# Kernel tuning notes

Hardware: AMD Instinct MI355X
Metric: run time of the kernel (lower is better)

The kernel has to match this reference:

```python
import jax, jax.numpy as jnp
import numpy as np

B, T, D = 2, 4096, 512
H = 8
HS = D // H  # 64
CTX = 4096


def setup_inputs() -> dict:
    key = jax.random.key(0)
    ks = jax.random.split(key, 10)
    s = lambda fan_in: fan_in ** -0.5
    x = jax.random.normal(ks[0], (B, T, D), dtype=jnp.float32)
    # per-head q/k/v projections (no bias), stacked over heads: [H, D, HS]
    Wq = jax.random.normal(ks[1], (H, D, HS), dtype=jnp.float32) * s(D)
    Wk = jax.random.normal(ks[2], (H, D, HS), dtype=jnp.float32) * s(D)
    Wv = jax.random.normal(ks[3], (H, D, HS), dtype=jnp.float32) * s(D)
    # output projection [D, D] + bias
    Wproj = jax.random.normal(ks[4], (D, D), dtype=jnp.float32) * s(D)
    bproj = jax.random.normal(ks[5], (D,), dtype=jnp.float32) * 0.01
    # feed-forward: D -> 4D -> D
    W1 = jax.random.normal(ks[6], (D, 4 * D), dtype=jnp.float32) * s(D)
    b1 = jax.random.normal(ks[7], (4 * D,), dtype=jnp.float32) * 0.01
    W2 = jax.random.normal(ks[8], (4 * D, D), dtype=jnp.float32) * s(4 * D)
    b2 = jax.random.normal(ks[9], (D,), dtype=jnp.float32) * 0.01
    return {"x": x, "Wq": Wq, "Wk": Wk, "Wv": Wv, "Wproj": Wproj,
            "bproj": bproj, "W1": W1, "b1": b1, "W2": W2, "b2": b2}


def reference(x, Wq, Wk, Wv, Wproj, bproj, W1, b1, W2, b2):
    Bx, Tx, Dx = x.shape
    scale = HS ** -0.5
    # multi-head causal self-attention (naive, full TxT scores as in source)
    q = jnp.einsum('btd,hde->bhte', x, Wq)
    k = jnp.einsum('btd,hde->bhte', x, Wk)
    v = jnp.einsum('btd,hde->bhte', x, Wv)
    wei = jnp.einsum('bhte,bhse->bhts', q, k) * scale  # [B,H,T,T]
    causal = jnp.tril(jnp.ones((Tx, Tx), dtype=bool))
    wei = jnp.where(causal, wei, -jnp.inf)
    wei = jax.nn.softmax(wei, axis=-1)
    attn = jnp.einsum('bhts,bhse->bhte', wei, v)  # [B,H,T,HS]
    # concat heads (cat along last dim == transpose+reshape of stacked heads)
    attn = attn.transpose(0, 2, 1, 3).reshape(Bx, Tx, Dx)
    sa_out = attn @ Wproj + bproj
    x = x + sa_out
    # feed-forward with residual
    h = jax.nn.relu(x @ W1 + b1)
    x = x + (h @ W2 + b2)
    return x
```

## Files before the change

kernel.cpp:

```cpp
#include <hip/hip_runtime.h>


typedef __attribute__((ext_vector_type(8))) short bf16x8;
typedef __attribute__((ext_vector_type(4))) float f32x4;
typedef __attribute__((ext_vector_type(16))) float f32x16;
typedef unsigned short u16;

__device__ __forceinline__ u16 f2bf(float f) {
  union { float f; unsigned int i; } u; u.f = f;
  unsigned int r = u.i + 0x7fffu + ((u.i >> 16) & 1u);
  return (u16)(r >> 16);
}
__device__ __forceinline__ float bf2f(u16 s) {
  union { unsigned int i; float f; } u; u.i = ((unsigned int)s) << 16;
  return u.f;
}
__device__ __forceinline__ void gload16(const void* g, void* l) {
  __builtin_amdgcn_global_load_lds((const __attribute__((address_space(1))) void*)g,
                                   (__attribute__((address_space(3))) void*)l,
                                   16, 0, 0);
}

__device__ __forceinline__ void plswap_u(unsigned &a, unsigned &b) {
#if defined(__has_builtin) && __has_builtin(__builtin_amdgcn_permlane32_swap)
  auto r = __builtin_amdgcn_permlane32_swap(a, b, false, false);
  a = (unsigned)r[0]; b = (unsigned)r[1];
#else
  asm("v_permlane32_swap_b32 %0, %1" : "+v"(a), "+v"(b));
#endif
}
__device__ __forceinline__ void plswap_f(float &a, float &b) {
  unsigned ua = __builtin_bit_cast(unsigned, a), ub = __builtin_bit_cast(unsigned, b);
  plswap_u(ua, ub);
  a = __builtin_bit_cast(float, ua); b = __builtin_bit_cast(float, ub);
}

__device__ __forceinline__ float tsum16(const f32x16 v) {
  float a = v[0] + v[8],  b = v[1] + v[9];
  float c = v[2] + v[10], d = v[3] + v[11];
  float e = v[4] + v[12], f = v[5] + v[13];
  float g = v[6] + v[14], h = v[7] + v[15];
  a += e; b += f; c += g; d += h;
  a += c; b += d;
  return a + b;
}

__global__ __launch_bounds__(256) void prep_kernel(
    const float* __restrict__ x, const float* __restrict__ Wq,
    const float* __restrict__ Wk, const float* __restrict__ Wv,
    const float* __restrict__ Wproj, const float* __restrict__ W1,
    const float* __restrict__ W2, ushort4* __restrict__ xb4,
    u16* __restrict__ wqkv_t, u16* __restrict__ wproj_t,
    u16* __restrict__ w1_t, u16* __restrict__ w2_t) {
  const int i = blockIdx.x;
  if (i >= 3072) {
    int idx = (i - 3072) * 256 + threadIdx.x;
    float4 v = ((const float4*)x)[idx];
    ushort4 o; o.x = f2bf(v.x); o.y = f2bf(v.y); o.z = f2bf(v.z); o.w = f2bf(v.w);
    xb4[idx] = o;
    return;
  }
  const float* in; u16* out; int C, ldo, bx, by;
  if (i < 768) {
    int which = i >> 8, r = i & 255;
    const float* W = which == 0 ? Wq : (which == 1 ? Wk : Wv);
    int bz = r >> 5;
    in = W + bz * 32768;
    out = wqkv_t + which * 262144 + bz * 32768;
    C = 64; ldo = 512; bx = r & 1; by = (r >> 1) & 15;
  } else if (i < 1024) {
    int r = i - 768;
    in = Wproj; out = wproj_t; C = 512; ldo = 512; bx = r & 15; by = r >> 4;
  } else if (i < 2048) {
    int r = i - 1024;
    in = W1; out = w1_t; C = 2048; ldo = 512; bx = r & 63; by = r >> 6;
  } else {
    int r = i - 2048;
    in = W2; out = w2_t; C = 512; ldo = 2048; bx = r & 15; by = r >> 4;
  }
  __shared__ float t[32][33];
  int c0 = bx * 32, r0 = by * 32;
  int tx = threadIdx.x & 31, ty = threadIdx.x >> 5;
#pragma unroll
  for (int k = 0; k < 4; k++)
    t[ty + 8 * k][tx] = in[(long)(r0 + ty + 8 * k) * C + c0 + tx];
  __syncthreads();
#pragma unroll
  for (int k = 0; k < 4; k++)
    out[(long)(c0 + ty + 8 * k) * ldo + r0 + tx] = f2bf(t[tx][ty + 8 * k]);
}

__global__ void transpose_v_kernel(const u16* __restrict__ qkv, u16* __restrict__ vt) {
  __shared__ u16 t[32][33];
  int z = blockIdx.z;
  const u16* in = qkv + (long)(z >> 3) * 4096 * 1536 + 1024 + (z & 7) * 64;
  u16* out = vt + (long)z * 64 * 4096;
  int c0 = blockIdx.x * 32, r0 = blockIdx.y * 32;
  int tx = threadIdx.x & 31, ty = threadIdx.x >> 5;
#pragma unroll
  for (int k = 0; k < 4; k++)
    t[ty + 8 * k][tx] = in[(long)(r0 + ty + 8 * k) * 1536 + c0 + tx];
  __syncthreads();
#pragma unroll
  for (int k = 0; k < 4; k++)
    out[(long)(c0 + ty + 8 * k) * 4096 + r0 + tx] = t[tx][ty + 8 * k];
}

template <int MODE, int BN>
__global__ __launch_bounds__(256) void gemm_bt_kernel(
    const u16* __restrict__ A, const u16* __restrict__ Bt, void* __restrict__ Out,
    const float* __restrict__ bias, const float* __restrict__ resf,
    const u16* __restrict__ resb, int N, int K) {
  __shared__ __align__(16) char As[128 * 128];
  __shared__ __align__(16) char Bs[BN * 128];
  const int tid = threadIdx.x;
  const int lane = tid & 63, w = tid >> 6;
  const int l15 = lane & 15, l4 = lane >> 4;
  const int nx = gridDim.x, nwg = nx * gridDim.y;
  int id = blockIdx.y * nx + blockIdx.x;
  id = (id & 7) * (nwg >> 3) + (id >> 3);
  const long m0 = (long)(id / nx) * 128;
  const long n0 = (long)(id % nx) * BN;
  const int wm = (w >> 1) * 64, wn = (w & 1) * (BN / 2);
  const int NB = BN / 32;

  f32x4 acc[4][NB] = {};

  for (int kt = 0; kt < K; kt += 64) {
#pragma unroll
    for (int i = 0; i < 4; i++) {
      int basechunk = i * 256 + w * 64;
      int chunk = basechunk + lane;
      int row = chunk >> 3, c = chunk & 7;
      int sc = c ^ (row & 7);
      gload16(A + (m0 + row) * K + kt + sc * 8, As + basechunk * 16);
    }
#pragma unroll
    for (int i = 0; i < BN / 32; i++) {
      int basechunk = i * 256 + w * 64;
      int chunk = basechunk + lane;
      int row = chunk >> 3, c = chunk & 7;
      int sc = c ^ (row & 7);
      gload16(Bt + (n0 + row) * K + kt + sc * 8, Bs + basechunk * 16);
    }
    __syncthreads();
#pragma unroll
    for (int kk = 0; kk < 2; kk++) {
      bf16x8 a[4], b[NB];
#pragma unroll
      for (int m = 0; m < 4; m++) {
        int row = wm + m * 16 + l15;
        int ch = (kk * 4 + l4) ^ (row & 7);
        a[m] = *(const bf16x8*)(As + row * 128 + ch * 16);
      }
#pragma unroll
      for (int n = 0; n < NB; n++) {
        int row = wn + n * 16 + l15;
        int ch = (kk * 4 + l4) ^ (row & 7);
        b[n] = *(const bf16x8*)(Bs + row * 128 + ch * 16);
      }
#pragma unroll
      for (int m = 0; m < 4; m++)
#pragma unroll
        for (int n = 0; n < NB; n++)
          acc[m][n] = __builtin_amdgcn_mfma_f32_16x16x32_bf16(a[m], b[n], acc[m][n], 0, 0, 0);
    }
    __syncthreads();
  }

#pragma unroll
  for (int m = 0; m < 4; m++) {
#pragma unroll
    for (int n = 0; n < NB; n++) {
      long gcol = n0 + wn + n * 16 + l15;
#pragma unroll
      for (int r = 0; r < 4; r++) {
        long grow = m0 + wm + m * 16 + l4 * 4 + r;
        float v = acc[m][n][r];
        if (MODE == 0) {
          ((u16*)Out)[grow * N + gcol] = f2bf(v);
        } else if (MODE == 1) {
          v += bias[gcol] + resf[grow * N + gcol];
          ((u16*)Out)[grow * N + gcol] = f2bf(v);
        } else if (MODE == 2) {
          v += bias[gcol];
          v = v > 0.f ? v : 0.f;
          ((u16*)Out)[grow * N + gcol] = f2bf(v);
        } else if (MODE == 3) {
          v += bias[gcol] + bf2f(resb[grow * N + gcol]);
          ((float*)Out)[grow * N + gcol] = v;
        } else {
          if (gcol < 512) v *= 0.18033688f;
          ((u16*)Out)[grow * N + gcol] = f2bf(v);
        }
      }
    }
  }
}

__global__ __launch_bounds__(512, 4) void attn_kernel(
    const u16* __restrict__ qkv, const u16* __restrict__ vt,
    u16* __restrict__ pacc, float* __restrict__ pli) {
  __shared__ __align__(16) char Ks[2][64 * 128];
  __shared__ __align__(16) char Vs[2][64 * 128];
  const int tid = threadIdx.x;
  const int lane = tid & 63, w = tid >> 6;
  const int l31 = lane & 31, l5 = lane >> 5;

  const int g = blockIdx.x;

  for (int it = 0; it < 2; ++it) {
    const int item = it ? 1023 - g : g;
    const int qt = item >> 6;
    const int bh = (item >> 2) & 15;
    const int qq = item & 3;
    const int b = bh >> 3, h = bh & 7;
    const int qt0 = qt * 256;
    const int L = qt + 1;
    const int j0 = qq * L, j1 = j0 + L;
    const int jdiag = 4 * qt;
    const u16* qbase = qkv + (long)b * 4096 * 1536 + h * 64;
    const u16* kbase = qbase + 512;
    const u16* vtbase = vt + (long)bh * 64 * 4096;

    const int qrow_g = qt0 + w * 32 + l31;
    bf16x8 aq[4];
    {
      const u16* qp = qbase + (long)qrow_g * 1536 + l5 * 8;
#pragma unroll
      for (int kk = 0; kk < 4; kk++) aq[kk] = *(const bf16x8*)(qp + kk * 16);
    }

    const int srow = tid >> 3, sc = (tid & 7) ^ (srow & 7);
    const u16* kp = kbase + (long)(j0 * 64 + srow) * 1536 + sc * 8;
    const u16* vp = vtbase + (long)srow * 4096 + j0 * 64 + sc * 8;
    gload16(kp, Ks[0] + w * 1024);
    gload16(vp, Vs[0] + w * 1024);
    __syncthreads();

    f32x16 oacc[2] = {};
    float li = 0.f;

    for (int j = j0; j < j1; ++j) {
      const int cur = (j - j0) & 1;
      if (j + 1 < j1) {
        kp += 64 * 1536;
        vp += 64;
        gload16(kp, Ks[cur ^ 1] + w * 1024);
        gload16(vp, Vs[cur ^ 1] + w * 1024);
      }

      const bool diag = (j >= jdiag);
      const int thr = qrow_g - j * 64;

#pragma unroll
      for (int n = 0; n < 2; n++) {
        f32x16 st = {};
        __builtin_amdgcn_s_setprio(1);
#pragma unroll
        for (int kk = 0; kk < 4; kk++) {
          int ch = ((l5 + 2 * kk) ^ (l31 & 7)) * 16;
          bf16x8 ak = *(const bf16x8*)(Ks[cur] + (n * 32 + l31) * 128 + ch);
          st = __builtin_amdgcn_mfma_f32_32x32x16_bf16(ak, aq[kk], st, 0, 0, 0);
        }
        __builtin_amdgcn_s_setprio(0);

        if (diag) {
#pragma unroll
          for (int reg = 0; reg < 16; reg++) {
            int key = n * 32 + 4 * l5 + (reg & 3) + 8 * (reg >> 2);
            if (key > thr) st[reg] = -1e30f;
          }
        }

#pragma unroll
        for (int reg = 0; reg < 16; reg++)
          st[reg] = exp2f(st[reg]);
        li += tsum16(st);

#pragma unroll
        for (int jj = 0; jj < 2; jj++) {
          unsigned w0, w1, w2, w3;
          {
            unsigned pa, pb;
            asm("v_cvt_pk_bf16_f32 %0, %1, %2" : "=v"(pa) : "v"(st[(2 * jj) * 4 + 0]), "v"(st[(2 * jj) * 4 + 1]));
            asm("v_cvt_pk_bf16_f32 %0, %1, %2" : "=v"(pb) : "v"(st[(2 * jj + 1) * 4 + 0]), "v"(st[(2 * jj + 1) * 4 + 1]));
            plswap_u(pa, pb);
            w0 = pa; w2 = pb;
          }
          {
            unsigned pa, pb;
            asm("v_cvt_pk_bf16_f32 %0, %1, %2" : "=v"(pa) : "v"(st[(2 * jj) * 4 + 2]), "v"(st[(2 * jj) * 4 + 3]));
            asm("v_cvt_pk_bf16_f32 %0, %1, %2" : "=v"(pb) : "v"(st[(2 * jj + 1) * 4 + 2]), "v"(st[(2 * jj + 1) * 4 + 3]));
            plswap_u(pa, pb);
            w1 = pa; w3 = pb;
          }
          union { unsigned u[4]; bf16x8 v; } bp;
          bp.u[0] = w0; bp.u[1] = w1; bp.u[2] = w2; bp.u[3] = w3;
          int s = 2 * n + jj;
          int ch = ((l5 + 2 * s) ^ (l31 & 7)) * 16;
          bf16x8 av0 = *(const bf16x8*)(Vs[cur] + l31 * 128 + ch);
          bf16x8 av1 = *(const bf16x8*)(Vs[cur] + (32 + l31) * 128 + ch);
          __builtin_amdgcn_s_setprio(1);
          oacc[0] = __builtin_amdgcn_mfma_f32_32x32x16_bf16(av0, bp.v, oacc[0], 0, 0, 0);
          oacc[1] = __builtin_amdgcn_mfma_f32_32x32x16_bf16(av1, bp.v, oacc[1], 0, 0, 0);
          __builtin_amdgcn_s_setprio(0);
        }
      }
      __syncthreads();
    }

    {
      float ta = li, tb = li;
      plswap_f(ta, tb);
      li = ta + tb;
    }

    u16* pa = pacc + (long)item * 16384;
#pragma unroll
    for (int ne = 0; ne < 2; ne++)
#pragma unroll
      for (int gg = 0; gg < 4; gg++) {
        ushort4 o;
        o.x = f2bf(oacc[ne][4 * gg + 0]);
        o.y = f2bf(oacc[ne][4 * gg + 1]);
        o.z = f2bf(oacc[ne][4 * gg + 2]);
        o.w = f2bf(oacc[ne][4 * gg + 3]);
        *(ushort4*)(pa + (w * 32 + l31) * 64 + ne * 32 + 4 * l5 + 8 * gg) = o;
      }
    if (l5 == 0) pli[(long)item * 256 + w * 32 + l31] = li;
  }
}

__global__ __launch_bounds__(256) void attn_merge_kernel(
    const u16* __restrict__ pacc, const float* __restrict__ pli, u16* __restrict__ attnb) {
  int tile = blockIdx.x;
  int qt = tile >> 4, bh = tile & 15;
  int b = bh >> 3, h = bh & 7;
  int ibase = qt * 64 + bh * 4;
  const u16* pq[4];
  const float* lq[4];
#pragma unroll
  for (int q = 0; q < 4; q++) {
    pq[q] = pacc + (long)(ibase + q) * 16384;
    lq[q] = pli + (long)(ibase + q) * 256;
  }
  int t = threadIdx.x;
  int cg = (t & 15) * 4;
  int rsub = t >> 4;
#pragma unroll
  for (int pass = 0; pass < 16; ++pass) {
    int row = pass * 16 + rsub;
    float denom = lq[0][row] + lq[1][row] + lq[2][row] + lq[3][row];
    float acc0 = 0.f, acc1 = 0.f, acc2 = 0.f, acc3 = 0.f;
#pragma unroll
    for (int q = 0; q < 4; q++) {
      ushort4 u = *(const ushort4*)(pq[q] + row * 64 + cg);
      acc0 += bf2f(u.x);
      acc1 += bf2f(u.y);
      acc2 += bf2f(u.z);
      acc3 += bf2f(u.w);
    }
    float inv = 1.f / denom;
    ushort4 o;
    o.x = f2bf(acc0 * inv);
    o.y = f2bf(acc1 * inv);
    o.z = f2bf(acc2 * inv);
    o.w = f2bf(acc3 * inv);
    *(ushort4*)(attnb + ((long)(b * 4096 + qt * 256 + row)) * 512 + h * 64 + cg) = o;
  }
}

extern "C" void kernel_launch(void* const* d_in, const int* in_sizes, int n_in,
                              void* d_out, int out_size, void* d_ws, size_t ws_size,
                              hipStream_t stream) {
  const float* x = (const float*)d_in[0];
  const float* Wq = (const float*)d_in[1];
  const float* Wk = (const float*)d_in[2];
  const float* Wv = (const float*)d_in[3];
  const float* Wproj = (const float*)d_in[4];
  const float* bproj = (const float*)d_in[5];
  const float* W1 = (const float*)d_in[6];
  const float* b1 = (const float*)d_in[7];
  const float* W2 = (const float*)d_in[8];
  const float* b2 = (const float*)d_in[9];

  char* ws = (char*)d_ws;
  u16* xb      = (u16*)(ws);
  u16* wqkv_t  = (u16*)(ws + 8388608);
  u16* wproj_t = (u16*)(ws + 9961472);
  u16* w1_t    = (u16*)(ws + 10485760);
  u16* w2_t    = (u16*)(ws + 12582912);
  u16* qkv     = (u16*)(ws + 14680064);
  u16* vt      = (u16*)(ws + 39845888);
  u16* attnb   = (u16*)(ws + 48234496);
  u16* x1b     = (u16*)(ws + 56623104);
  u16* hbuf    = (u16*)(ws + 65011712);
  float* pli   = (float*)(ws + 56623104 + 2097152);
  u16* pacc    = (u16*)(ws + 65011712);

  prep_kernel<<<7168, 256, 0, stream>>>(x, Wq, Wk, Wv, Wproj, W1, W2,
                                        (ushort4*)xb, wqkv_t, wproj_t, w1_t, w2_t);

  gemm_bt_kernel<4, 128><<<dim3(12, 64), 256, 0, stream>>>(xb, wqkv_t, qkv, nullptr, nullptr, nullptr, 1536, 512);
  transpose_v_kernel<<<dim3(2, 128, 16), 256, 0, stream>>>(qkv, vt);
  attn_kernel<<<512, 512, 0, stream>>>(qkv, vt, pacc, pli);
  attn_merge_kernel<<<256, 256, 0, stream>>>(pacc, pli, attnb);
  gemm_bt_kernel<1, 64><<<dim3(8, 64), 256, 0, stream>>>(attnb, wproj_t, x1b, bproj, x, nullptr, 512, 512);
  gemm_bt_kernel<2, 128><<<dim3(16, 64), 256, 0, stream>>>(x1b, w1_t, hbuf, b1, nullptr, nullptr, 2048, 512);
  gemm_bt_kernel<3, 64><<<dim3(8, 64), 256, 0, stream>>>(hbuf, w2_t, d_out, b2, nullptr, x1b, 512, 2048);
}
```

Baseline: 184.5 us.

## Fuse V transpose into QKV GEMM epilogue and launch one attention item per block

The QKV GEMM epilogue now writes V columns directly in transposed per-head layout, so the separate transpose_v kernel launch and its extra read/write pass over V go away. The attention kernel now launches 1024 blocks with one work item each instead of 512 blocks looping over two paired items. The block-to-item mapping interleaves long and short query tiles for load balance. The V stores in the GEMM epilogue are strided across rows, which may be less coalesced than the old tiled transpose.

Measured after the change: 193.6 us. 4.9% more time.

```diff
diff --git a/kernel.cpp b/kernel.cpp
--- a/kernel.cpp
+++ b/kernel.cpp
@@ -90,27 +90,11 @@
     out[(long)(c0 + ty + 8 * k) * ldo + r0 + tx] = f2bf(t[tx][ty + 8 * k]);
 }
 
-__global__ void transpose_v_kernel(const u16* __restrict__ qkv, u16* __restrict__ vt) {
-  __shared__ u16 t[32][33];
-  int z = blockIdx.z;
-  const u16* in = qkv + (long)(z >> 3) * 4096 * 1536 + 1024 + (z & 7) * 64;
-  u16* out = vt + (long)z * 64 * 4096;
-  int c0 = blockIdx.x * 32, r0 = blockIdx.y * 32;
-  int tx = threadIdx.x & 31, ty = threadIdx.x >> 5;
-#pragma unroll
-  for (int k = 0; k < 4; k++)
-    t[ty + 8 * k][tx] = in[(long)(r0 + ty + 8 * k) * 1536 + c0 + tx];
-  __syncthreads();
-#pragma unroll
-  for (int k = 0; k < 4; k++)
-    out[(long)(c0 + ty + 8 * k) * 4096 + r0 + tx] = t[tx][ty + 8 * k];
-}
-
 template <int MODE, int BN>
 __global__ __launch_bounds__(256) void gemm_bt_kernel(
     const u16* __restrict__ A, const u16* __restrict__ Bt, void* __restrict__ Out,
     const float* __restrict__ bias, const float* __restrict__ resf,
-    const u16* __restrict__ resb, int N, int K) {
+    const u16* __restrict__ resb, u16* __restrict__ vtOut, int N, int K) {
   __shared__ __align__(16) char As[128 * 128];
   __shared__ __align__(16) char Bs[BN * 128];
   const int tid = threadIdx.x;
@@ -173,25 +157,43 @@
 #pragma unroll
     for (int n = 0; n < NB; n++) {
       long gcol = n0 + wn + n * 16 + l15;
-#pragma unroll
-      for (int r = 0; r < 4; r++) {
-        long grow = m0 + wm + m * 16 + l4 * 4 + r;
-        float v = acc[m][n][r];
-        if (MODE == 0) {
-          ((u16*)Out)[grow * N + gcol] = f2bf(v);
-        } else if (MODE == 1) {
-          v += bias[gcol] + resf[grow * N + gcol];
-          ((u16*)Out)[grow * N + gcol] = f2bf(v);
-        } else if (MODE == 2) {
-          v += bias[gcol];
-          v = v > 0.f ? v : 0.f;
-          ((u16*)Out)[grow * N + gcol] = f2bf(v);
-        } else if (MODE == 3) {
-          v += bias[gcol] + bf2f(resb[grow * N + gcol]);
-          ((float*)Out)[grow * N + gcol] = v;
+      if (MODE == 4) {
+        long grow0 = m0 + wm + m * 16 + l4 * 4;
+        if (gcol < 1024) {
+          const float s = (gcol < 512) ? 0.18033688f : 1.0f;
+#pragma unroll
+          for (int r = 0; r < 4; r++)
+            ((u16*)Out)[(grow0 + r) * N + gcol] = f2bf(acc[m][n][r] * s);
         } else {
-          if (gcol < 512) v *= 0.18033688f;
-          ((u16*)Out)[grow * N + gcol] = f2bf(v);
+          int bb = (int)(grow0 >> 12);
+          long trow0 = grow0 & 4095;
+          int hc = (int)(gcol - 1024);
+          int bhh = bb * 8 + (hc >> 6), e = hc & 63;
+          ushort4 o;
+          o.x = f2bf(acc[m][n][0]);
+          o.y = f2bf(acc[m][n][1]);
+          o.z = f2bf(acc[m][n][2]);
+          o.w = f2bf(acc[m][n][3]);
+          *(ushort4*)(vtOut + (long)bhh * 262144 + (long)e * 4096 + trow0) = o;
+        }
+      } else {
+#pragma unroll
+        for (int r = 0; r < 4; r++) {
+          long grow = m0 + wm + m * 16 + l4 * 4 + r;
+          float v = acc[m][n][r];
+          if (MODE == 0) {
+            ((u16*)Out)[grow * N + gcol] = f2bf(v);
+          } else if (MODE == 1) {
+            v += bias[gcol] + resf[grow * N + gcol];
+            ((u16*)Out)[grow * N + gcol] = f2bf(v);
+          } else if (MODE == 2) {
+            v += bias[gcol];
+            v = v > 0.f ? v : 0.f;
+            ((u16*)Out)[grow * N + gcol] = f2bf(v);
+          } else {
+            v += bias[gcol] + bf2f(resb[grow * N + gcol]);
+            ((float*)Out)[grow * N + gcol] = v;
+          }
         }
       }
     }
@@ -208,128 +210,126 @@
   const int l31 = lane & 31, l5 = lane >> 5;
 
   const int g = blockIdx.x;
-
-  for (int it = 0; it < 2; ++it) {
-    const int item = it ? 1023 - g : g;
-    const int qt = item >> 6;
-    const int bh = (item >> 2) & 15;
-    const int qq = item & 3;
-    const int b = bh >> 3, h = bh & 7;
-    const int qt0 = qt * 256;
-    const int L = qt + 1;
-    const int j0 = qq * L, j1 = j0 + L;
-    const int jdiag = 4 * qt;
-    const u16* qbase = qkv + (long)b * 4096 * 1536 + h * 64;
-    const u16* kbase = qbase + 512;
-    const u16* vtbase = vt + (long)bh * 64 * 4096;
-
-    const int qrow_g = qt0 + w * 32 + l31;
-    bf16x8 aq[4];
-    {
-      const u16* qp = qbase + (long)qrow_g * 1536 + l5 * 8;
-#pragma unroll
-      for (int kk = 0; kk < 4; kk++) aq[kk] = *(const bf16x8*)(qp + kk * 16);
-    }
-
-    const int srow = tid >> 3, sc = (tid & 7) ^ (srow & 7);
-    const u16* kp = kbase + (long)(j0 * 64 + srow) * 1536 + sc * 8;
-    const u16* vp = vtbase + (long)srow * 4096 + j0 * 64 + sc * 8;
-    gload16(kp, Ks[0] + w * 1024);
-    gload16(vp, Vs[0] + w * 1024);
+  const int s_ = g >> 8, r_ = g & 255, t_ = r_ >> 4, u_ = r_ & 15;
+  const int qt = (s_ & 1) ? 15 - t_ : t_;
+  const int sub = (s_ << 4) | u_;
+  const int item = qt * 64 + sub;
+  const int bh = sub >> 2, qq = sub & 3;
+  const int b = bh >> 3, h = bh & 7;
+  const int qt0 = qt * 256;
+  const int L = qt + 1;
+  const int j0 = qq * L, j1 = j0 + L;
+  const int jdiag = 4 * qt;
+  const u16* qbase = qkv + (long)b * 4096 * 1536 + h * 64;
+  const u16* kbase = qbase + 512;
+  const u16* vtbase = vt + (long)bh * 64 * 4096;
+
+  const int qrow_g = qt0 + w * 32 + l31;
+  bf16x8 aq[4];
+  {
+    const u16* qp = qbase + (long)qrow_g * 1536 + l5 * 8;
+#pragma unroll
+    for (int kk = 0; kk < 4; kk++) aq[kk] = *(const bf16x8*)(qp + kk * 16);
+  }
+
+  const int srow = tid >> 3, sc = (tid & 7) ^ (srow & 7);
+  const u16* kp = kbase + (long)(j0 * 64 + srow) * 1536 + sc * 8;
+  const u16* vp = vtbase + (long)srow * 4096 + j0 * 64 + sc * 8;
+  gload16(kp, Ks[0] + w * 1024);
+  gload16(vp, Vs[0] + w * 1024);
+  __syncthreads();
+
+  f32x16 oacc[2] = {};
+  float li = 0.f;
+
+  for (int j = j0; j < j1; ++j) {
+    const int cur = (j - j0) & 1;
+    if (j + 1 < j1) {
+      kp += 64 * 1536;
+      vp += 64;
+      gload16(kp, Ks[cur ^ 1] + w * 1024);
+      gload16(vp, Vs[cur ^ 1] + w * 1024);
+    }
+
+    const bool diag = (j >= jdiag);
+    const int thr = qrow_g - j * 64;
+
+#pragma unroll
+    for (int n = 0; n < 2; n++) {
+      f32x16 st = {};
+      __builtin_amdgcn_s_setprio(1);
+#pragma unroll
+      for (int kk = 0; kk < 4; kk++) {
+        int ch = ((l5 + 2 * kk) ^ (l31 & 7)) * 16;
+        bf16x8 ak = *(const bf16x8*)(Ks[cur] + (n * 32 + l31) * 128 + ch);
+        st = __builtin_amdgcn_mfma_f32_32x32x16_bf16(ak, aq[kk], st, 0, 0, 0);
+      }
+      __builtin_amdgcn_s_setprio(0);
+
+      if (diag) {
+#pragma unroll
+        for (int reg = 0; reg < 16; reg++) {
+          int key = n * 32 + 4 * l5 + (reg & 3) + 8 * (reg >> 2);
+          if (key > thr) st[reg] = -1e30f;
+        }
+      }
+
+#pragma unroll
+      for (int reg = 0; reg < 16; reg++)
+        st[reg] = exp2f(st[reg]);
+      li += tsum16(st);
+
+#pragma unroll
+      for (int jj = 0; jj < 2; jj++) {
+        unsigned w0, w1, w2, w3;
+        {
+          unsigned pa, pb;
+          asm("v_cvt_pk_bf16_f32 %0, %1, %2" : "=v"(pa) : "v"(st[(2 * jj) * 4 + 0]), "v"(st[(2 * jj) * 4 + 1]));
+          asm("v_cvt_pk_bf16_f32 %0, %1, %2" : "=v"(pb) : "v"(st[(2 * jj + 1) * 4 + 0]), "v"(st[(2 * jj + 1) * 4 + 1]));
+          plswap_u(pa, pb);
+          w0 = pa; w2 = pb;
+        }
+        {
+          unsigned pa, pb;
+          asm("v_cvt_pk_bf16_f32 %0, %1, %2" : "=v"(pa) : "v"(st[(2 * jj) * 4 + 2]), "v"(st[(2 * jj) * 4 + 3]));
+          asm("v_cvt_pk_bf16_f32 %0, %1, %2" : "=v"(pb) : "v"(st[(2 * jj + 1) * 4 + 2]), "v"(st[(2 * jj + 1) * 4 + 3]));
+          plswap_u(pa, pb);
+          w1 = pa; w3 = pb;
+        }
+        union { unsigned u[4]; bf16x8 v; } bp;
+        bp.u[0] = w0; bp.u[1] = w1; bp.u[2] = w2; bp.u[3] = w3;
+        int s2 = 2 * n + jj;
+        int ch = ((l5 + 2 * s2) ^ (l31 & 7)) * 16;
+        bf16x8 av0 = *(const bf16x8*)(Vs[cur] + l31 * 128 + ch);
+        bf16x8 av1 = *(const bf16x8*)(Vs[cur] + (32 + l31) * 128 + ch);
+        __builtin_amdgcn_s_setprio(1);
+        oacc[0] = __builtin_amdgcn_mfma_f32_32x32x16_bf16(av0, bp.v, oacc[0], 0, 0, 0);
+        oacc[1] = __builtin_amdgcn_mfma_f32_32x32x16_bf16(av1, bp.v, oacc[1], 0, 0, 0);
+        __builtin_amdgcn_s_setprio(0);
+      }
+    }
     __syncthreads();
-
-    f32x16 oacc[2] = {};
-    float li = 0.f;
-
-    for (int j = j0; j < j1; ++j) {
-      const int cur = (j - j0) & 1;
-      if (j + 1 < j1) {
-        kp += 64 * 1536;
-        vp += 64;
-        gload16(kp, Ks[cur ^ 1] + w * 1024);
-        gload16(vp, Vs[cur ^ 1] + w * 1024);
-      }
-
-      const bool diag = (j >= jdiag);
-      const int thr = qrow_g - j * 64;
-
-#pragma unroll
-      for (int n = 0; n < 2; n++) {
-        f32x16 st = {};
-        __builtin_amdgcn_s_setprio(1);
-#pragma unroll
-        for (int kk = 0; kk < 4; kk++) {
-          int ch = ((l5 + 2 * kk) ^ (l31 & 7)) * 16;
-          bf16x8 ak = *(const bf16x8*)(Ks[cur] + (n * 32 + l31) * 128 + ch);
-          st = __builtin_amdgcn_mfma_f32_32x32x16_bf16(ak, aq[kk], st, 0, 0, 0);
-        }
-        __builtin_amdgcn_s_setprio(0);
-
-        if (diag) {
-#pragma unroll
-          for (int reg = 0; reg < 16; reg++) {
-            int key = n * 32 + 4 * l5 + (reg & 3) + 8 * (reg >> 2);
-            if (key > thr) st[reg] = -1e30f;
-          }
-        }
-
-#pragma unroll
-        for (int reg = 0; reg < 16; reg++)
-          st[reg] = exp2f(st[reg]);
-        li += tsum16(st);
-
-#pragma unroll
-        for (int jj = 0; jj < 2; jj++) {
-          unsigned w0, w1, w2, w3;
-          {
-            unsigned pa, pb;
-            asm("v_cvt_pk_bf16_f32 %0, %1, %2" : "=v"(pa) : "v"(st[(2 * jj) * 4 + 0]), "v"(st[(2 * jj) * 4 + 1]));
-            asm("v_cvt_pk_bf16_f32 %0, %1, %2" : "=v"(pb) : "v"(st[(2 * jj + 1) * 4 + 0]), "v"(st[(2 * jj + 1) * 4 + 1]));
-            plswap_u(pa, pb);
-            w0 = pa; w2 = pb;
-          }
-          {
-            unsigned pa, pb;
-            asm("v_cvt_pk_bf16_f32 %0, %1, %2" : "=v"(pa) : "v"(st[(2 * jj) * 4 + 2]), "v"(st[(2 * jj) * 4 + 3]));
-            asm("v_cvt_pk_bf16_f32 %0, %1, %2" : "=v"(pb) : "v"(st[(2 * jj + 1) * 4 + 2]), "v"(st[(2 * jj + 1) * 4 + 3]));
-            plswap_u(pa, pb);
-            w1 = pa; w3 = pb;
-          }
-          union { unsigned u[4]; bf16x8 v; } bp;
-          bp.u[0] = w0; bp.u[1] = w1; bp.u[2] = w2; bp.u[3] = w3;
-          int s = 2 * n + jj;
-          int ch = ((l5 + 2 * s) ^ (l31 & 7)) * 16;
-          bf16x8 av0 = *(const bf16x8*)(Vs[cur] + l31 * 128 + ch);
-          bf16x8 av1 = *(const bf16x8*)(Vs[cur] + (32 + l31) * 128 + ch);
-          __builtin_amdgcn_s_setprio(1);
-          oacc[0] = __builtin_amdgcn_mfma_f32_32x32x16_bf16(av0, bp.v, oacc[0], 0, 0, 0);
-          oacc[1] = __builtin_amdgcn_mfma_f32_32x32x16_bf16(av1, bp.v, oacc[1], 0, 0, 0);
-          __builtin_amdgcn_s_setprio(0);
-        }
-      }
-      __syncthreads();
-    }
-
-    {
-      float ta = li, tb = li;
-      plswap_f(ta, tb);
-      li = ta + tb;
-    }
-
-    u16* pa = pacc + (long)item * 16384;
-#pragma unroll
-    for (int ne = 0; ne < 2; ne++)
-#pragma unroll
-      for (int gg = 0; gg < 4; gg++) {
-        ushort4 o;
-        o.x = f2bf(oacc[ne][4 * gg + 0]);
-        o.y = f2bf(oacc[ne][4 * gg + 1]);
-        o.z = f2bf(oacc[ne][4 * gg + 2]);
-        o.w = f2bf(oacc[ne][4 * gg + 3]);
-        *(ushort4*)(pa + (w * 32 + l31) * 64 + ne * 32 + 4 * l5 + 8 * gg) = o;
-      }
-    if (l5 == 0) pli[(long)item * 256 + w * 32 + l31] = li;
-  }
+  }
+
+  {
+    float ta = li, tb = li;
+    plswap_f(ta, tb);
+    li = ta + tb;
+  }
+
+  u16* pa = pacc + (long)item * 16384;
+#pragma unroll
+  for (int ne = 0; ne < 2; ne++)
+#pragma unroll
+    for (int gg = 0; gg < 4; gg++) {
+      ushort4 o;
+      o.x = f2bf(oacc[ne][4 * gg + 0]);
+      o.y = f2bf(oacc[ne][4 * gg + 1]);
+      o.z = f2bf(oacc[ne][4 * gg + 2]);
+      o.w = f2bf(oacc[ne][4 * gg + 3]);
+      *(ushort4*)(pa + (w * 32 + l31) * 64 + ne * 32 + 4 * l5 + 8 * gg) = o;
+    }
+  if (l5 == 0) pli[(long)item * 256 + w * 32 + l31] = li;
 }
 
 __global__ __launch_bounds__(256) void attn_merge_kernel(
@@ -402,11 +402,10 @@
   prep_kernel<<<7168, 256, 0, stream>>>(x, Wq, Wk, Wv, Wproj, W1, W2,
                                         (ushort4*)xb, wqkv_t, wproj_t, w1_t, w2_t);
 
-  gemm_bt_kernel<4, 128><<<dim3(12, 64), 256, 0, stream>>>(xb, wqkv_t, qkv, nullptr, nullptr, nullptr, 1536, 512);
-  transpose_v_kernel<<<dim3(2, 128, 16), 256, 0, stream>>>(qkv, vt);
-  attn_kernel<<<512, 512, 0, stream>>>(qkv, vt, pacc, pli);
+  gemm_bt_kernel<4, 128><<<dim3(12, 64), 256, 0, stream>>>(xb, wqkv_t, qkv, nullptr, nullptr, nullptr, vt, 1536, 512);
+  attn_kernel<<<1024, 512, 0, stream>>>(qkv, vt, pacc, pli);
   attn_merge_kernel<<<256, 256, 0, stream>>>(pacc, pli, attnb);
-  gemm_bt_kernel<1, 64><<<dim3(8, 64), 256, 0, stream>>>(attnb, wproj_t, x1b, bproj, x, nullptr, 512, 512);
-  gemm_bt_kernel<2, 128><<<dim3(16, 64), 256, 0, stream>>>(x1b, w1_t, hbuf, b1, nullptr, nullptr, 2048, 512);
-  gemm_bt_kernel<3, 64><<<dim3(8, 64), 256, 0, stream>>>(hbuf, w2_t, d_out, b2, nullptr, x1b, 512, 2048);
-}
+  gemm_bt_kernel<1, 64><<<dim3(8, 64), 256, 0, stream>>>(attnb, wproj_t, x1b, bproj, x, nullptr, nullptr, 512, 512);
+  gemm_bt_kernel<2, 128><<<dim3(16, 64), 256, 0, stream>>>(x1b, w1_t, hbuf, b1, nullptr, nullptr, nullptr, 2048, 512);
+  gemm_bt_kernel<3, 64><<<dim3(8, 64), 256, 0, stream>>>(hbuf, w2_t, d_out, b2, nullptr, x1b, nullptr, 512, 2048);
+}
```
